# Performance work log

Hardware: AMD Instinct MI355X
Metric: run time of the kernel (lower is better)

The kernel has to match this reference:

```python
import jax, jax.numpy as jnp
import numpy as np

# Complete A-ary tree of depth D, nodes stored in level order.
# Children of node i are A*i+1 .. A*i+A.
B, A, D = 512, 4, 6
N = (A**D - 1) // (A - 1)  # 1365 nodes per tree
V, E_EMB, E_ENC = 50000, 128, 128


def setup_inputs() -> dict:
    key = jax.random.key(0)
    ks = jax.random.split(key, 5)
    tokens = jax.random.randint(ks[0], (B, N), 0, V)
    emb = jax.random.normal(ks[1], (V, E_EMB), jnp.float32) * 0.02
    Wc_W = jax.random.normal(ks[2], (E_ENC, E_EMB), jnp.float32) / np.sqrt(E_EMB)
    Wc_b = jnp.zeros((E_ENC,), jnp.float32)
    Ws_W = jax.random.normal(ks[3], (E_ENC, E_ENC), jnp.float32) / np.sqrt(E_ENC)
    Ws_b = jnp.zeros((E_ENC,), jnp.float32)
    return {"tokens": tokens, "emb": emb, "Wc_W": Wc_W, "Wc_b": Wc_b,
            "Ws_W": Ws_W, "Ws_b": Ws_b, "bs": B}


def reference(tokens, emb, Wc_W, Wc_b, Ws_W, Ws_b, bs):
    # Per-node local term: W_c(embedding(token))  -> [B, N, E]
    e = emb[tokens] @ Wc_W.T + Wc_b
    level_sizes = [A ** d for d in range(D)]
    starts = np.cumsum([0] + level_sizes)  # static offsets into level order

    # Bottom-up recurrence: h(node) = e(node) + sum_children W_sum(h(child)).
    # W_sum (incl. bias) is applied per child then summed, matching the
    # per-child-slot index_copy + Linear in the original recursion.
    hs = [None] * D
    hs[D - 1] = e[:, starts[D - 1]:starts[D]]  # leaves
    for d in range(D - 2, -1, -1):
        child = hs[d + 1]                        # [B, A^(d+1), E]
        proj = child @ Ws_W.T + Ws_b             # W_sum per child
        agg = proj.reshape(bs, level_sizes[d], A, E_ENC).sum(axis=2)
        hs[d] = e[:, starts[d]:starts[d + 1]] + agg

    h_all = jnp.concatenate(hs, axis=1)          # [B, N, E]
    # node_list holds activation(h) per tree position; combine = max over nodes
    return jnp.max(jax.nn.relu(h_all), axis=1)   # [B, E]
```

## Files before the change

### kernel.cpp

```cpp
#include <hip/hip_runtime.h>
#include <hip/hip_bf16.h>

#define NTOK 1365
#define ED   128
#define STR  136
#define VROWS 50000
#define PROWS 50048

typedef __attribute__((ext_vector_type(8))) short short8;
typedef __attribute__((ext_vector_type(4))) float f32x4;

#define MFMA(a,b,c) __builtin_amdgcn_mfma_f32_16x16x32_bf16((a),(b),(c),0,0,0)

__device__ __forceinline__ ushort f2bf(float f) {
  union { float f; unsigned u; } v; v.f = f;
  unsigned r = v.u + 0x7fffu + ((v.u >> 16) & 1u);
  return (ushort)(r >> 16);
}
__device__ __forceinline__ ushort4 cvt4(float4 f) {
  ushort4 u; u.x = f2bf(f.x); u.y = f2bf(f.y); u.z = f2bf(f.z); u.w = f2bf(f.w);
  return u;
}
__device__ __forceinline__ short8 pack8(float4 a, float4 b) {
  union { ushort us[8]; short8 s8; } t;
  t.us[0]=f2bf(a.x); t.us[1]=f2bf(a.y); t.us[2]=f2bf(a.z); t.us[3]=f2bf(a.w);
  t.us[4]=f2bf(b.x); t.us[5]=f2bf(b.y); t.us[6]=f2bf(b.z); t.us[7]=f2bf(b.w);
  return t.s8;
}

__global__ __attribute__((amdgpu_flat_work_group_size(256, 256)))
void proj_kernel(const float* __restrict__ emb, const float* __restrict__ WcW,
                 const float* __restrict__ Wcb, ushort* __restrict__ P) {
  const int tid = threadIdx.x, w = tid >> 6, lane = tid & 63;
  const int n16 = lane & 15, quad = lane >> 4, kof = quad * 8;
  const int m0 = blockIdx.x * 64;

  float bv[2];
  short8 Bp[2][4];
  #pragma unroll
  for (int j = 0; j < 2; j++) {
    const int c = w*32 + j*16 + n16;
    bv[j] = Wcb[c];
    #pragma unroll
    for (int kb = 0; kb < 4; kb++) {
      const float* pc = WcW + c*ED + kb*32 + kof;
      Bp[j][kb] = pack8(((const float4*)pc)[0], ((const float4*)pc)[1]);
    }
  }
  #pragma unroll
  for (int i = 0; i < 4; i++) {
    int arow = m0 + i*16 + n16; if (arow >= VROWS) arow = 0;
    f32x4 acc0 = (f32x4){0.f,0.f,0.f,0.f}, acc1 = (f32x4){0.f,0.f,0.f,0.f};
    #pragma unroll
    for (int kb = 0; kb < 4; kb++) {
      const float* pa = emb + (long)arow*ED + kb*32 + kof;
      short8 a = pack8(((const float4*)pa)[0], ((const float4*)pa)[1]);
      acc0 = MFMA(a, Bp[0][kb], acc0);
      acc1 = MFMA(a, Bp[1][kb], acc1);
    }
    #pragma unroll
    for (int r = 0; r < 4; r++) {
      const int orow = m0 + i*16 + quad*4 + r;
      if (orow < VROWS) {
        P[(long)orow*ED + w*32 + n16]      = f2bf(acc0[r] + bv[0]);
        P[(long)orow*ED + w*32 + 16 + n16] = f2bf(acc1[r] + bv[1]);
      }
    }
  }
}

#define SMP_BYTES (4096 + 276 * STR * 2)

__global__ __attribute__((amdgpu_flat_work_group_size(512, 512),
                          amdgpu_waves_per_eu(4, 8)))
void tree_kernel_p(
    const int* __restrict__ tokens, const ushort* __restrict__ P,
    const float* __restrict__ WsW,  const float* __restrict__ Wsb,
    float* __restrict__ out) {
  extern __shared__ char smem[];
  float*  PM  = (float*)smem;
  ushort* Xe0 = (ushort*)(PM + 1024);
  ushort* Xe1 = Xe0 + 64*STR;
  ushort* CS4 = Xe1 + 64*STR;
  ushort* CS3 = CS4 + 64*STR;
  ushort* CS2 = CS3 + 64*STR;
  ushort* CS1 = CS2 + 16*STR;

  const int  tid = threadIdx.x;
  const int  b   = blockIdx.x;
  const long tokbase = (long)b * NTOK;
  const int  w    = tid >> 6;
  const int  lane = tid & 63;
  const int  n16  = lane & 15;
  const int  quad = lane >> 4;
  const int  mtg  = w >> 2, ntg = w & 3;
  const int  kof  = quad * 8;

  float bsv[2];
  #pragma unroll
  for (int j = 0; j < 2; j++) bsv[j] = 4.f * Wsb[ntg*32 + j*16 + n16];

  short8 Bs[2][4];
  #pragma unroll
  for (int jt = 0; jt < 2; jt++)
    #pragma unroll
    for (int kb = 0; kb < 4; kb++) {
      const float* pc = WsW + (ntg*32 + jt*16 + n16)*ED + kb*32 + kof;
      Bs[jt][kb] = pack8(((const float4*)pc)[0], ((const float4*)pc)[1]);
    }

  short8 I2[2];
  #pragma unroll
  for (int j = 0; j < 2; j++) {
    union { ushort us[8]; short8 s8; } t;
    #pragma unroll
    for (int e = 0; e < 8; e++) t.us[e] = 0;
    if (quad == 2*j + (n16 >> 3)) t.us[n16 & 7] = 0x3F80;
    I2[j] = t.s8;
  }

  for (int i = tid; i < 1024; i += 512) PM[i] = 0.f;
  float pm[2] = {0.f, 0.f};

  short8 RA[2], RB[2];
  auto issue64 = [&](short8 (&R)[2], int ofs) {
    const int r = tid >> 3, p = tid & 7;
    const short8* src = (const short8*)(P + (long)tokens[tokbase + ofs + r]*ED) + (p << 1);
    R[0] = src[0]; R[1] = src[1];
  };
  auto store64 = [&](const short8 (&R)[2], ushort* Xe) {
    const int r = tid >> 3, p = tid & 7;
    short8* d = (short8*)(Xe + r*STR + (p << 4));
    d[0] = R[0]; d[1] = R[1];
  };
  auto issueN = [&](short8 (&R)[2], int ofs, int nrows) {
    const int r = tid >> 5, p = tid & 31;
    if (r < nrows) {
      ushort4 v = *((const ushort4*)(P + (long)tokens[tokbase + ofs + r]*ED) + p);
      R[0][0] = (short)v.x; R[0][1] = (short)v.y;
      R[0][2] = (short)v.z; R[0][3] = (short)v.w;
    }
  };
  auto storeN = [&](const short8 (&R)[2], ushort* Xe, int nrows) {
    const int r = tid >> 5, p = tid & 31;
    if (r < nrows) {
      ushort4 v; v.x = (ushort)R[0][0]; v.y = (ushort)R[0][1];
      v.z = (ushort)R[0][2]; v.w = (ushort)R[0][3];
      *(ushort4*)(Xe + r*STR + (p << 2)) = v;
    }
  };

  auto phase64 = [&](const ushort* Xe, const ushort* csrc, ushort* csdst, int csrow0) {
    f32x4 acc[2][2];
    #pragma unroll
    for (int i = 0; i < 2; i++)
      #pragma unroll
      for (int j = 0; j < 2; j++) acc[i][j] = (f32x4){0.f,0.f,0.f,0.f};
    {
      const int ko = ntg*32 + kof;
      short8 a0 = *(const short8*)(Xe + (mtg*32      + n16)*STR + ko);
      short8 a1 = *(const short8*)(Xe + (mtg*32 + 16 + n16)*STR + ko);
      acc[0][0]=MFMA(a0,I2[0],acc[0][0]); acc[0][1]=MFMA(a0,I2[1],acc[0][1]);
      acc[1][0]=MFMA(a1,I2[0],acc[1][0]); acc[1][1]=MFMA(a1,I2[1],acc[1][1]);
    }
    if (csrc) {
      #pragma unroll
      for (int kb = 0; kb < 4; kb++) {
        const int ko = kb*32 + kof;
        short8 c0 = *(const short8*)(csrc + (mtg*32      + n16)*STR + ko);
        short8 c1 = *(const short8*)(csrc + (mtg*32 + 16 + n16)*STR + ko);
        acc[0][0]=MFMA(c0,Bs[0][kb],acc[0][0]); acc[0][1]=MFMA(c0,Bs[1][kb],acc[0][1]);
        acc[1][0]=MFMA(c1,Bs[0][kb],acc[1][0]); acc[1][1]=MFMA(c1,Bs[1][kb],acc[1][1]);
      }
    }
    #pragma unroll
    for (int i = 0; i < 2; i++) {
      const int p = mtg*8 + i*4 + quad;
      #pragma unroll
      for (int j = 0; j < 2; j++) {
        const float bb = csrc ? bsv[j] : 0.f;
        f32x4 A = acc[i][j];
        float h0=A[0]+bb, h1=A[1]+bb, h2=A[2]+bb, h3=A[3]+bb;
        pm[j] = fmaxf(pm[j], fmaxf(fmaxf(h0,h1), fmaxf(h2,h3)));
        csdst[(csrow0 + p)*STR + ntg*32 + j*16 + n16] =
            f2bf(A[0]+A[1]+A[2]+A[3] + 4.f*bb);
      }
    }
  };

  auto smallphase = [&](const ushort* Xe, const ushort* csrc, int M, ushort* csdst) {
    if (mtg != 0) return;
    const int ar = (M == 16) ? n16 : ((M == 4) ? (n16 & 3) : 0);
    f32x4 acc[2];
    acc[0] = (f32x4){0.f,0.f,0.f,0.f}; acc[1] = (f32x4){0.f,0.f,0.f,0.f};
    {
      const int ko = ntg*32 + kof;
      short8 a = *(const short8*)(Xe + ar*STR + ko);
      acc[0] = MFMA(a, I2[0], acc[0]); acc[1] = MFMA(a, I2[1], acc[1]);
    }
    #pragma unroll
    for (int kb = 0; kb < 4; kb++) {
      const int ko = kb*32 + kof;
      short8 c2 = *(const short8*)(csrc + ar*STR + ko);
      acc[0] = MFMA(c2, Bs[0][kb], acc[0]); acc[1] = MFMA(c2, Bs[1][kb], acc[1]);
    }
    #pragma unroll
    for (int j = 0; j < 2; j++) {
      const float bb = bsv[j];
      f32x4 A = acc[j];
      const int c = ntg*32 + j*16 + n16;
      if (M == 16) {
        float h0=A[0]+bb, h1=A[1]+bb, h2=A[2]+bb, h3=A[3]+bb;
        pm[j] = fmaxf(pm[j], fmaxf(fmaxf(h0,h1), fmaxf(h2,h3)));
        csdst[quad*STR + c] = f2bf(A[0]+A[1]+A[2]+A[3] + 4.f*bb);
      } else if (M == 4) {
        if (quad == 0) {
          float h0=A[0]+bb, h1=A[1]+bb, h2=A[2]+bb, h3=A[3]+bb;
          pm[j] = fmaxf(pm[j], fmaxf(fmaxf(h0,h1), fmaxf(h2,h3)));
          csdst[c] = f2bf(A[0]+A[1]+A[2]+A[3] + 4.f*bb);
        }
      } else {
        if (quad == 0) pm[j] = fmaxf(pm[j], A[0] + bb);
      }
    }
  };

  issue64(RA, 341);
  issue64(RB, 341 + 64);
  store64(RA, Xe0);
  __syncthreads();
   issue64(RA, 341+128);     phase64(Xe0, nullptr, CS4,  0); store64(RB, Xe1); __syncthreads();
   issue64(RB, 341+192);     phase64(Xe1, nullptr, CS4, 16); store64(RA, Xe0); __syncthreads();
   issue64(RA, 85);          phase64(Xe0, nullptr, CS4, 32); store64(RB, Xe1); __syncthreads();
   issue64(RB, 341+256);     phase64(Xe1, nullptr, CS4, 48); store64(RA, Xe0); __syncthreads();
   issue64(RA, 341+256+64);  phase64(Xe0, CS4,     CS3,  0); store64(RB, Xe1); __syncthreads();
   issue64(RB, 341+256+128); phase64(Xe1, nullptr, CS4,  0); store64(RA, Xe0); __syncthreads();
   issue64(RA, 341+256+192); phase64(Xe0, nullptr, CS4, 16); store64(RB, Xe1); __syncthreads();
   issue64(RB, 85+64);       phase64(Xe1, nullptr, CS4, 32); store64(RA, Xe0); __syncthreads();
   issue64(RA, 341+512);     phase64(Xe0, nullptr, CS4, 48); store64(RB, Xe1); __syncthreads();
   issue64(RB, 341+512+64);  phase64(Xe1, CS4,     CS3, 16); store64(RA, Xe0); __syncthreads();
   issue64(RA, 341+512+128); phase64(Xe0, nullptr, CS4,  0); store64(RB, Xe1); __syncthreads();
   issue64(RB, 341+512+192); phase64(Xe1, nullptr, CS4, 16); store64(RA, Xe0); __syncthreads();
   issue64(RA, 85+128);      phase64(Xe0, nullptr, CS4, 32); store64(RB, Xe1); __syncthreads();
   issue64(RB, 341+768);     phase64(Xe1, nullptr, CS4, 48); store64(RA, Xe0); __syncthreads();
   issue64(RA, 341+768+64);  phase64(Xe0, CS4,     CS3, 32); store64(RB, Xe1); __syncthreads();
   issue64(RB, 341+768+128); phase64(Xe1, nullptr, CS4,  0); store64(RA, Xe0); __syncthreads();
   issue64(RA, 341+768+192); phase64(Xe0, nullptr, CS4, 16); store64(RB, Xe1); __syncthreads();
   issue64(RB, 85+192);      phase64(Xe1, nullptr, CS4, 32); store64(RA, Xe0); __syncthreads();
   issue64(RA, 21);          phase64(Xe0, nullptr, CS4, 48); store64(RB, Xe1); __syncthreads();
   issueN(RB, 5, 16);        phase64(Xe1, CS4,     CS3, 48); store64(RA, Xe0); __syncthreads();
   issueN(RA, 1, 4);         phase64(Xe0, CS3,     CS2,  0); storeN(RB, Xe1, 16); __syncthreads();
   issueN(RB, 0, 1);         smallphase(Xe1, CS2, 16, CS1);  storeN(RA, Xe0, 4);  __syncthreads();
                             smallphase(Xe0, CS1, 4,  CS2);  storeN(RB, Xe1, 1);  __syncthreads();
                             smallphase(Xe1, CS2, 1,  nullptr);

  #pragma unroll
  for (int j = 0; j < 2; j++) {
    float v = pm[j];
    v = fmaxf(v, __shfl_xor(v, 16, 64));
    v = fmaxf(v, __shfl_xor(v, 32, 64));
    if (quad == 0) PM[w*128 + ntg*32 + j*16 + n16] = v;
  }
  __syncthreads();
  if (tid < 128) {
    float m = 0.f;
    #pragma unroll
    for (int r = 0; r < 8; r++) m = fmaxf(m, PM[r*128 + tid]);
    out[(long)b*ED + tid] = m;
  }
}

#define SM_BYTES (4096 + 404 * STR * 2)

__global__ __attribute__((amdgpu_flat_work_group_size(512, 512),
                          amdgpu_waves_per_eu(2, 8)))
void tree_kernel(
    const int* __restrict__ tokens, const float* __restrict__ emb,
    const float* __restrict__ WcW,  const float* __restrict__ Wcb,
    const float* __restrict__ WsW,  const float* __restrict__ Wsb,
    float* __restrict__ out) {
  extern __shared__ char smem[];
  float*  PM  = (float*)smem;
  ushort* WsL = (ushort*)(PM + 1024);
  ushort* Xe0 = WsL + 128*STR;
  ushort* Xe1 = Xe0 + 64*STR;
  ushort* CS4 = Xe1 + 64*STR;
  ushort* CS3 = CS4 + 64*STR;
  ushort* CS2 = CS3 + 64*STR;
  ushort* CS1 = CS2 + 16*STR;

  const int  tid = threadIdx.x;
  const int  b   = blockIdx.x;
  const long tokbase = (long)b * NTOK;
  const int  w    = tid >> 6;
  const int  lane = tid & 63;
  const int  n16  = lane & 15;
  const int  quad = lane >> 4;
  const int  mtg  = w >> 2, ntg = w & 3;
  const int  kof  = quad * 8;

  float bcv[2], bsv[2];
  #pragma unroll
  for (int j = 0; j < 2; j++) {
    const int c = ntg*32 + j*16 + n16;
    bcv[j] = Wcb[c]; bsv[j] = 4.f * Wsb[c];
  }

  short8 Bc[2][4];
  #pragma unroll
  for (int jt = 0; jt < 2; jt++)
    #pragma unroll
    for (int kb = 0; kb < 4; kb++) {
      const float* pc = WcW + (ntg*32 + jt*16 + n16)*ED + kb*32 + kof;
      Bc[jt][kb] = pack8(((const float4*)pc)[0], ((const float4*)pc)[1]);
    }

  #pragma unroll
  for (int i = 0; i < 8; i++) {
    const int idx = tid + i*512;
    float4 f = ((const float4*)WsW)[idx];
    *(ushort4*)(WsL + (idx >> 5)*STR + ((idx & 31) << 2)) = cvt4(f);
  }

  for (int i = tid; i < 1024; i += 512) PM[i] = 0.f;
  float pm[2] = {0.f, 0.f};

  float4 RA[4], RB[4];
  auto issue64 = [&](float4 (&R)[4], int ofs) {
    const int r = tid >> 3, p = tid & 7;
    const float4* src = (const float4*)(emb + (long)tokens[tokbase + ofs + r]*ED) + (p << 2);
    R[0] = src[0]; R[1] = src[1]; R[2] = src[2]; R[3] = src[3];
  };
  auto store64 = [&](const float4 (&R)[4], ushort* Xe) {
    const int r = tid >> 3, p = tid & 7;
    short8* d = (short8*)(Xe + r*STR + (p << 4));
    d[0] = pack8(R[0], R[1]); d[1] = pack8(R[2], R[3]);
  };
  auto issueN = [&](float4 (&R)[4], int ofs, int nrows) {
    const int r = tid >> 5, p = tid & 31;
    if (r < nrows) R[0] = ((const float4*)(emb + (long)tokens[tokbase + ofs + r]*ED))[p];
  };
  auto storeN = [&](const float4 (&R)[4], ushort* Xe, int nrows) {
    const int r = tid >> 5, p = tid & 31;
    if (r < nrows) *(ushort4*)(Xe + r*STR + (p << 2)) = cvt4(R[0]);
  };

  auto phase64 = [&](const ushort* Xe, const ushort* csrc, ushort* csdst, int csrow0) {
    f32x4 acc[2][2];
    #pragma unroll
    for (int i = 0; i < 2; i++)
      #pragma unroll
      for (int j = 0; j < 2; j++) acc[i][j] = (f32x4){0.f,0.f,0.f,0.f};
    #pragma unroll
    for (int kb = 0; kb < 4; kb++) {
      const int ko = kb*32 + kof;
      short8 a0 = *(const short8*)(Xe + (mtg*32      + n16)*STR + ko);
      short8 a1 = *(const short8*)(Xe + (mtg*32 + 16 + n16)*STR + ko);
      acc[0][0]=MFMA(a0,Bc[0][kb],acc[0][0]); acc[0][1]=MFMA(a0,Bc[1][kb],acc[0][1]);
      acc[1][0]=MFMA(a1,Bc[0][kb],acc[1][0]); acc[1][1]=MFMA(a1,Bc[1][kb],acc[1][1]);
      if (csrc) {
        short8 c0 = *(const short8*)(csrc + (mtg*32      + n16)*STR + ko);
        short8 c1 = *(const short8*)(csrc + (mtg*32 + 16 + n16)*STR + ko);
        short8 s0 = *(const short8*)(WsL  + (ntg*32      + n16)*STR + ko);
        short8 s1 = *(const short8*)(WsL  + (ntg*32 + 16 + n16)*STR + ko);
        acc[0][0]=MFMA(c0,s0,acc[0][0]); acc[0][1]=MFMA(c0,s1,acc[0][1]);
        acc[1][0]=MFMA(c1,s0,acc[1][0]); acc[1][1]=MFMA(c1,s1,acc[1][1]);
      }
    }
    #pragma unroll
    for (int i = 0; i < 2; i++) {
      const int p = mtg*8 + i*4 + quad;
      #pragma unroll
      for (int j = 0; j < 2; j++) {
        const float bb = csrc ? (bcv[j] + bsv[j]) : bcv[j];
        f32x4 A = acc[i][j];
        float h0=A[0]+bb, h1=A[1]+bb, h2=A[2]+bb, h3=A[3]+bb;
        pm[j] = fmaxf(pm[j], fmaxf(fmaxf(h0,h1), fmaxf(h2,h3)));
        csdst[(csrow0 + p)*STR + ntg*32 + j*16 + n16] =
            f2bf(A[0]+A[1]+A[2]+A[3] + 4.f*bb);
      }
    }
  };

  auto smallphase = [&](const ushort* Xe, const ushort* csrc, int M, ushort* csdst) {
    if (mtg != 0) return;
    const int ar = (M == 16) ? n16 : ((M == 4) ? (n16 & 3) : 0);
    f32x4 acc[2];
    acc[0] = (f32x4){0.f,0.f,0.f,0.f}; acc[1] = (f32x4){0.f,0.f,0.f,0.f};
    #pragma unroll
    for (int kb = 0; kb < 4; kb++) {
      const int ko = kb*32 + kof;
      short8 a  = *(const short8*)(Xe   + ar*STR + ko);
      short8 c2 = *(const short8*)(csrc + ar*STR + ko);
      short8 s0 = *(const short8*)(WsL + (ntg*32      + n16)*STR + ko);
      short8 s1 = *(const short8*)(WsL + (ntg*32 + 16 + n16)*STR + ko);
      acc[0] = MFMA(a,  Bc[0][kb], acc[0]); acc[1] = MFMA(a,  Bc[1][kb], acc[1]);
      acc[0] = MFMA(c2, s0, acc[0]);        acc[1] = MFMA(c2, s1, acc[1]);
    }
    #pragma unroll
    for (int j = 0; j < 2; j++) {
      const float bb = bcv[j] + bsv[j];
      f32x4 A = acc[j];
      const int c = ntg*32 + j*16 + n16;
      if (M == 16) {
        float h0=A[0]+bb, h1=A[1]+bb, h2=A[2]+bb, h3=A[3]+bb;
        pm[j] = fmaxf(pm[j], fmaxf(fmaxf(h0,h1), fmaxf(h2,h3)));
        csdst[quad*STR + c] = f2bf(A[0]+A[1]+A[2]+A[3] + 4.f*bb);
      } else if (M == 4) {
        if (quad == 0) {
          float h0=A[0]+bb, h1=A[1]+bb, h2=A[2]+bb, h3=A[3]+bb;
          pm[j] = fmaxf(pm[j], fmaxf(fmaxf(h0,h1), fmaxf(h2,h3)));
          csdst[c] = f2bf(A[0]+A[1]+A[2]+A[3] + 4.f*bb);
        }
      } else {
        if (quad == 0) pm[j] = fmaxf(pm[j], A[0] + bb);
      }
    }
  };

  issue64(RA, 341);
  issue64(RB, 341 + 64);
  store64(RA, Xe0);
  __syncthreads();
  issue64(RA, 341+128);     phase64(Xe0, nullptr, CS4,  0); store64(RB, Xe1); __syncthreads();
  issue64(RB, 341+192);     phase64(Xe1, nullptr, CS4, 16); store64(RA, Xe0); __syncthreads();
  issue64(RA, 85);          phase64(Xe0, nullptr, CS4, 32); store64(RB, Xe1); __syncthreads();
  issue64(RB, 341+256);     phase64(Xe1, nullptr, CS4, 48); store64(RA, Xe0); __syncthreads();
  issue64(RA, 341+256+64);  phase64(Xe0, CS4,     CS3,  0); store64(RB, Xe1); __syncthreads();
  issue64(RB, 341+256+128); phase64(Xe1, nullptr, CS4,  0); store64(RA, Xe0); __syncthreads();
  issue64(RA, 341+256+192); phase64(Xe0, nullptr, CS4, 16); store64(RB, Xe1); __syncthreads();
  issue64(RB, 85+64);       phase64(Xe1, nullptr, CS4, 32); store64(RA, Xe0); __syncthreads();
  issue64(RA, 341+512);     phase64(Xe0, nullptr, CS4, 48); store64(RB, Xe1); __syncthreads();
  issue64(RB, 341+512+64);  phase64(Xe1, CS4,     CS3, 16); store64(RA, Xe0); __syncthreads();
  issue64(RA, 341+512+128); phase64(Xe0, nullptr, CS4,  0); store64(RB, Xe1); __syncthreads();
  issue64(RB, 341+512+192); phase64(Xe1, nullptr, CS4, 16); store64(RA, Xe0); __syncthreads();
  issue64(RA, 85+128);      phase64(Xe0, nullptr, CS4, 32); store64(RB, Xe1); __syncthreads();
  issue64(RB, 341+768);     phase64(Xe1, nullptr, CS4, 48); store64(RA, Xe0); __syncthreads();
  issue64(RA, 341+768+64);  phase64(Xe0, CS4,     CS3, 32); store64(RB, Xe1); __syncthreads();
  issue64(RB, 341+768+128); phase64(Xe1, nullptr, CS4,  0); store64(RA, Xe0); __syncthreads();
  issue64(RA, 341+768+192); phase64(Xe0, nullptr, CS4, 16); store64(RB, Xe1); __syncthreads();
  issue64(RB, 85+192);      phase64(Xe1, nullptr, CS4, 32); store64(RA, Xe0); __syncthreads();
  issue64(RA, 21);          phase64(Xe0, nullptr, CS4, 48); store64(RB, Xe1); __syncthreads();
  issueN(RB, 5, 16);        phase64(Xe1, CS4,     CS3, 48); store64(RA, Xe0); __syncthreads();
  issueN(RA, 1, 4);         phase64(Xe0, CS3,     CS2,  0); storeN(RB, Xe1, 16); __syncthreads();
  issueN(RB, 0, 1);         smallphase(Xe1, CS2, 16, CS1);  storeN(RA, Xe0, 4);  __syncthreads();
                            smallphase(Xe0, CS1, 4,  CS2);  storeN(RB, Xe1, 1);  __syncthreads();
                            smallphase(Xe1, CS2, 1,  nullptr);

  #pragma unroll
  for (int j = 0; j < 2; j++) {
    float v = pm[j];
    v = fmaxf(v, __shfl_xor(v, 16, 64));
    v = fmaxf(v, __shfl_xor(v, 32, 64));
    if (quad == 0) PM[w*128 + ntg*32 + j*16 + n16] = v;
  }
  __syncthreads();
  if (tid < 128) {
    float m = 0.f;
    #pragma unroll
    for (int r = 0; r < 8; r++) m = fmaxf(m, PM[r*128 + tid]);
    out[(long)b*ED + tid] = m;
  }
}

extern "C" void kernel_launch(void* const* d_in, const int* in_sizes, int n_in,
                              void* d_out, int out_size, void* d_ws, size_t ws_size,
                              hipStream_t stream) {
  const int*   tokens = (const int*)d_in[0];
  const float* emb    = (const float*)d_in[1];
  const float* WcW    = (const float*)d_in[2];
  const float* Wcb    = (const float*)d_in[3];
  const float* WsW    = (const float*)d_in[4];
  const float* Wsb    = (const float*)d_in[5];
  float* out = (float*)d_out;

  const size_t needP = (size_t)PROWS * ED * sizeof(ushort);
  if (d_ws != nullptr && ws_size >= needP) {
    ushort* P = (ushort*)d_ws;
    proj_kernel<<<(VROWS + 63) / 64, 256, 0, stream>>>(emb, WcW, Wcb, P);
    hipFuncSetAttribute(reinterpret_cast<const void*>(tree_kernel_p),
                        hipFuncAttributeMaxDynamicSharedMemorySize, SMP_BYTES);
    tree_kernel_p<<<512, 512, SMP_BYTES, stream>>>(tokens, P, WsW, Wsb, out);
  } else {
    hipFuncSetAttribute(reinterpret_cast<const void*>(tree_kernel),
                        hipFuncAttributeMaxDynamicSharedMemorySize, SM_BYTES);
    tree_kernel<<<512, 512, SM_BYTES, stream>>>(tokens, emb, WcW, Wcb, WsW, Wsb, out);
  }
}
```

Baseline: 135.3 us.

## Stage tokens and embedding tiles in LDS, use lighter barriers that skip vmcnt waits

The tree kernel now preloads all 1365 token indices for its tree into shared memory, so the gather address for each row comes from LDS instead of a dependent global load. The pipeline barriers are replaced with a custom barrier that waits only on LDS operations, which lets the prefetched global gathers stay in flight across barriers. The proj kernel stages the embedding tile into LDS as bf16 with coalesced loads before the MFMA loop, and PM is moved to alias CS4 to free shared memory. The custom barrier depends on a compiler inline-asm ordering, and the PM aliasing depends on CS4 being dead at the point it is zeroed.

```diff
diff --git a/kernel.cpp b/kernel.cpp
--- a/kernel.cpp
+++ b/kernel.cpp
@@ -12,6 +12,10 @@
 
 #define MFMA(a,b,c) __builtin_amdgcn_mfma_f32_16x16x32_bf16((a),(b),(c),0,0,0)
 
+#define BAR() do { asm volatile("s_waitcnt lgkmcnt(0)" ::: "memory"); \
+                   __builtin_amdgcn_s_barrier();                      \
+                   asm volatile("" ::: "memory"); } while (0)
+
 __device__ __forceinline__ ushort f2bf(float f) {
   union { float f; unsigned u; } v; v.f = f;
   unsigned r = v.u + 0x7fffu + ((v.u >> 16) & 1u);
@@ -31,10 +35,20 @@
 __global__ __attribute__((amdgpu_flat_work_group_size(256, 256)))
 void proj_kernel(const float* __restrict__ emb, const float* __restrict__ WcW,
                  const float* __restrict__ Wcb, ushort* __restrict__ P) {
+  __shared__ ushort At[64 * STR];
   const int tid = threadIdx.x, w = tid >> 6, lane = tid & 63;
   const int n16 = lane & 15, quad = lane >> 4, kof = quad * 8;
   const int m0 = blockIdx.x * 64;
 
+  #pragma unroll
+  for (int i = 0; i < 8; i++) {
+    const int idx = tid + i*256;
+    const int r = idx >> 5, c4 = idx & 31;
+    int arow = m0 + r; if (arow >= VROWS) arow = 0;
+    float4 f = ((const float4*)(emb + (long)arow*ED))[c4];
+    *(ushort4*)(At + r*STR + (c4 << 2)) = cvt4(f);
+  }
+
   float bv[2];
   short8 Bp[2][4];
   #pragma unroll
@@ -47,14 +61,14 @@
       Bp[j][kb] = pack8(((const float4*)pc)[0], ((const float4*)pc)[1]);
     }
   }
+  __syncthreads();
+
   #pragma unroll
   for (int i = 0; i < 4; i++) {
-    int arow = m0 + i*16 + n16; if (arow >= VROWS) arow = 0;
     f32x4 acc0 = (f32x4){0.f,0.f,0.f,0.f}, acc1 = (f32x4){0.f,0.f,0.f,0.f};
     #pragma unroll
     for (int kb = 0; kb < 4; kb++) {
-      const float* pa = emb + (long)arow*ED + kb*32 + kof;
-      short8 a = pack8(((const float4*)pa)[0], ((const float4*)pa)[1]);
+      short8 a = *(const short8*)(At + (i*16 + n16)*STR + kb*32 + kof);
       acc0 = MFMA(a, Bp[0][kb], acc0);
       acc1 = MFMA(a, Bp[1][kb], acc1);
     }
@@ -69,7 +83,8 @@
   }
 }
 
-#define SMP_BYTES (4096 + 276 * STR * 2)
+#define TKB 5472
+#define SMP_BYTES (TKB + 276 * STR * 2)
 
 __global__ __attribute__((amdgpu_flat_work_group_size(512, 512),
                           amdgpu_waves_per_eu(4, 8)))
@@ -78,17 +93,17 @@
     const float* __restrict__ WsW,  const float* __restrict__ Wsb,
     float* __restrict__ out) {
   extern __shared__ char smem[];
-  float*  PM  = (float*)smem;
-  ushort* Xe0 = (ushort*)(PM + 1024);
+  int*    TK  = (int*)smem;
+  ushort* Xe0 = (ushort*)(smem + TKB);
   ushort* Xe1 = Xe0 + 64*STR;
   ushort* CS4 = Xe1 + 64*STR;
   ushort* CS3 = CS4 + 64*STR;
   ushort* CS2 = CS3 + 64*STR;
   ushort* CS1 = CS2 + 16*STR;
+  float*  PM  = (float*)CS4;
 
   const int  tid = threadIdx.x;
   const int  b   = blockIdx.x;
-  const long tokbase = (long)b * NTOK;
   const int  w    = tid >> 6;
   const int  lane = tid & 63;
   const int  n16  = lane & 15;
@@ -96,6 +111,11 @@
   const int  mtg  = w >> 2, ntg = w & 3;
   const int  kof  = quad * 8;
 
+  {
+    const long tokbase = (long)b * NTOK;
+    for (int i = tid; i < NTOK; i += 512) TK[i] = tokens[tokbase + i];
+  }
+
   float bsv[2];
   #pragma unroll
   for (int j = 0; j < 2; j++) bsv[j] = 4.f * Wsb[ntg*32 + j*16 + n16];
@@ -119,13 +139,12 @@
     I2[j] = t.s8;
   }
 
-  for (int i = tid; i < 1024; i += 512) PM[i] = 0.f;
   float pm[2] = {0.f, 0.f};
 
   short8 RA[2], RB[2];
   auto issue64 = [&](short8 (&R)[2], int ofs) {
     const int r = tid >> 3, p = tid & 7;
-    const short8* src = (const short8*)(P + (long)tokens[tokbase + ofs + r]*ED) + (p << 1);
+    const short8* src = (const short8*)(P + (long)TK[ofs + r]*ED) + (p << 1);
     R[0] = src[0]; R[1] = src[1];
   };
   auto store64 = [&](const short8 (&R)[2], ushort* Xe) {
@@ -136,7 +155,7 @@
   auto issueN = [&](short8 (&R)[2], int ofs, int nrows) {
     const int r = tid >> 5, p = tid & 31;
     if (r < nrows) {
-      ushort4 v = *((const ushort4*)(P + (long)tokens[tokbase + ofs + r]*ED) + p);
+      ushort4 v = *((const ushort4*)(P + (long)TK[ofs + r]*ED) + p);
       R[0][0] = (short)v.x; R[0][1] = (short)v.y;
       R[0][2] = (short)v.z; R[0][3] = (short)v.w;
     }
@@ -225,33 +244,36 @@
     }
   };
 
+  __syncthreads();
   issue64(RA, 341);
   issue64(RB, 341 + 64);
   store64(RA, Xe0);
-  __syncthreads();
-   issue64(RA, 341+128);     phase64(Xe0, nullptr, CS4,  0); store64(RB, Xe1); __syncthreads();
-   issue64(RB, 341+192);     phase64(Xe1, nullptr, CS4, 16); store64(RA, Xe0); __syncthreads();
-   issue64(RA, 85);          phase64(Xe0, nullptr, CS4, 32); store64(RB, Xe1); __syncthreads();
-   issue64(RB, 341+256);     phase64(Xe1, nullptr, CS4, 48); store64(RA, Xe0); __syncthreads();
-   issue64(RA, 341+256+64);  phase64(Xe0, CS4,     CS3,  0); store64(RB, Xe1); __syncthreads();
-   issue64(RB, 341+256+128); phase64(Xe1, nullptr, CS4,  0); store64(RA, Xe0); __syncthreads();
-   issue64(RA, 341+256+192); phase64(Xe0, nullptr, CS4, 16); store64(RB, Xe1); __syncthreads();
-   issue64(RB, 85+64);       phase64(Xe1, nullptr, CS4, 32); store64(RA, Xe0); __syncthreads();
-   issue64(RA, 341+512);     phase64(Xe0, nullptr, CS4, 48); store64(RB, Xe1); __syncthreads();
-   issue64(RB, 341+512+64);  phase64(Xe1, CS4,     CS3, 16); store64(RA, Xe0); __syncthreads();
-   issue64(RA, 341+512+128); phase64(Xe0, nullptr, CS4,  0); store64(RB, Xe1); __syncthreads();
-   issue64(RB, 341+512+192); phase64(Xe1, nullptr, CS4, 16); store64(RA, Xe0); __syncthreads();
-   issue64(RA, 85+128);      phase64(Xe0, nullptr, CS4, 32); store64(RB, Xe1); __syncthreads();
-   issue64(RB, 341+768);     phase64(Xe1, nullptr, CS4, 48); store64(RA, Xe0); __syncthreads();
-   issue64(RA, 341+768+64);  phase64(Xe0, CS4,     CS3, 32); store64(RB, Xe1); __syncthreads();
-   issue64(RB, 341+768+128); phase64(Xe1, nullptr, CS4,  0); store64(RA, Xe0); __syncthreads();
-   issue64(RA, 341+768+192); phase64(Xe0, nullptr, CS4, 16); store64(RB, Xe1); __syncthreads();
-   issue64(RB, 85+192);      phase64(Xe1, nullptr, CS4, 32); store64(RA, Xe0); __syncthreads();
-   issue64(RA, 21);          phase64(Xe0, nullptr, CS4, 48); store64(RB, Xe1); __syncthreads();
-   issueN(RB, 5, 16);        phase64(Xe1, CS4,     CS3, 48); store64(RA, Xe0); __syncthreads();
-   issueN(RA, 1, 4);         phase64(Xe0, CS3,     CS2,  0); storeN(RB, Xe1, 16); __syncthreads();
-   issueN(RB, 0, 1);         smallphase(Xe1, CS2, 16, CS1);  storeN(RA, Xe0, 4);  __syncthreads();
-                             smallphase(Xe0, CS1, 4,  CS2);  storeN(RB, Xe1, 1);  __syncthreads();
+  BAR();
+   issue64(RA, 341+128);     phase64(Xe0, nullptr, CS4,  0); store64(RB, Xe1); BAR();
+   issue64(RB, 341+192);     phase64(Xe1, nullptr, CS4, 16); store64(RA, Xe0); BAR();
+   issue64(RA, 85);          phase64(Xe0, nullptr, CS4, 32); store64(RB, Xe1); BAR();
+   issue64(RB, 341+256);     phase64(Xe1, nullptr, CS4, 48); store64(RA, Xe0); BAR();
+   issue64(RA, 341+256+64);  phase64(Xe0, CS4,     CS3,  0); store64(RB, Xe1); BAR();
+   issue64(RB, 341+256+128); phase64(Xe1, nullptr, CS4,  0); store64(RA, Xe0); BAR();
+   issue64(RA, 341+256+192); phase64(Xe0, nullptr, CS4, 16); store64(RB, Xe1); BAR();
+   issue64(RB, 85+64);       phase64(Xe1, nullptr, CS4, 32); store64(RA, Xe0); BAR();
+   issue64(RA, 341+512);     phase64(Xe0, nullptr, CS4, 48); store64(RB, Xe1); BAR();
+   issue64(RB, 341+512+64);  phase64(Xe1, CS4,     CS3, 16); store64(RA, Xe0); BAR();
+   issue64(RA, 341+512+128); phase64(Xe0, nullptr, CS4,  0); store64(RB, Xe1); BAR();
+   issue64(RB, 341+512+192); phase64(Xe1, nullptr, CS4, 16); store64(RA, Xe0); BAR();
+   issue64(RA, 85+128);      phase64(Xe0, nullptr, CS4, 32); store64(RB, Xe1); BAR();
+   issue64(RB, 341+768);     phase64(Xe1, nullptr, CS4, 48); store64(RA, Xe0); BAR();
+   issue64(RA, 341+768+64);  phase64(Xe0, CS4,     CS3, 32); store64(RB, Xe1); BAR();
+   issue64(RB, 341+768+128); phase64(Xe1, nullptr, CS4,  0); store64(RA, Xe0); BAR();
+   issue64(RA, 341+768+192); phase64(Xe0, nullptr, CS4, 16); store64(RB, Xe1); BAR();
+   issue64(RB, 85+192);      phase64(Xe1, nullptr, CS4, 32); store64(RA, Xe0); BAR();
+   issue64(RA, 21);          phase64(Xe0, nullptr, CS4, 48); store64(RB, Xe1); BAR();
+   issueN(RB, 5, 16);        phase64(Xe1, CS4,     CS3, 48); store64(RA, Xe0); BAR();
+  issueN(RA, 1, 4);                  phase64(Xe0, CS3,     CS2,  0);
+  for (int i = tid; i < 1024; i += 512) PM[i] = 0.f;
+  storeN(RB, Xe1, 16); BAR();
+   issueN(RB, 0, 1);         smallphase(Xe1, CS2, 16, CS1);  storeN(RA, Xe0, 4);  BAR();
+                             smallphase(Xe0, CS1, 4,  CS2);  storeN(RB, Xe1, 1);  BAR();
                              smallphase(Xe1, CS2, 1,  nullptr);
 
   #pragma unroll
```

After: 360.5 us. 2.67x slower.
